# Kernel tuning notes

Measured on AMD Instinct MI355X. Metric: run time of the kernel, lower is better.

Reference implementation:

```python
import jax, jax.numpy as jnp
import numpy as np

B, KLEN, QLEN = 16, 4096, 1
D_MODEL, HEADS, KERNELS = 1024, 8, 10
DIM = D_MODEL // HEADS  # 128
SCALE = 0.02


def setup_inputs() -> dict:
    key = jax.random.key(0)
    ks = jax.random.split(key, 12)
    return {
        "query": jax.random.normal(ks[0], (B, QLEN, D_MODEL), jnp.float32),
        "key_in": jax.random.normal(ks[1], (B, KLEN, D_MODEL), jnp.float32),
        "value": jax.random.normal(ks[2], (B, KLEN, D_MODEL), jnp.float32),
        "prev_align": jax.random.uniform(ks[3], (B, HEADS, KLEN), jnp.float32),
        # learned params
        "conv_w": jax.random.normal(ks[4], (KERNELS, HEADS, 3), jnp.float32) * SCALE,   # OIH, k=3
        "conv_b": jnp.zeros((KERNELS,), jnp.float32),
        "w_u": jax.random.normal(ks[5], (KERNELS, DIM), jnp.float32) * SCALE,
        "w_q": jax.random.normal(ks[6], (D_MODEL, HEADS * DIM), jnp.float32) * SCALE,
        "w_v": jax.random.normal(ks[7], (D_MODEL, HEADS * DIM), jnp.float32) * SCALE,
        "bias": jax.random.uniform(ks[8], (DIM,), jnp.float32, minval=-0.1, maxval=0.1),
        "score_w": jax.random.normal(ks[9], (DIM,), jnp.float32) * SCALE,
        "score_b": jnp.zeros((), jnp.float32),
    }


def reference(query, key_in, value, prev_align, conv_w, conv_b, w_u, w_q, w_v, bias, score_w, score_b):
    b, k_len = key_in.shape[0], key_in.shape[1]
    # location features: conv1d over k_len with heads as channels -> [B, KERNELS, k_len]
    loc = jax.lax.conv_general_dilated(
        prev_align, conv_w, window_strides=(1,), padding=[(1, 1)],
        dimension_numbers=("NCH", "OIH", "NCH")) + conv_b[None, :, None]
    loc_energy = jnp.tanh(jnp.einsum("bck,cd->bkd", loc, w_u))  # [B, k_len, DIM]
    # projections split into heads
    q = jnp.einsum("bqf,fe->bqe", query, w_q).reshape(b, QLEN, HEADS, DIM).transpose(0, 2, 1, 3)   # [B,H,1,DIM]
    k = jnp.einsum("bkf,fe->bke", key_in, w_v).reshape(b, k_len, HEADS, DIM).transpose(0, 2, 1, 3)  # [B,H,K,DIM]
    v = value.reshape(b, k_len, HEADS, DIM).transpose(0, 2, 1, 3)                                   # [B,H,K,DIM]
    # additive energy (q_len==1 broadcasts over keys)
    e = jnp.tanh(k + q + loc_energy[:, None] + bias)            # [B,H,K,DIM]
    score = jnp.einsum("bhkd,d->bhk", e, score_w) + score_b    # [B,H,K]
    align = jax.nn.softmax(score, axis=-1)
    context = jnp.einsum("bhk,bhkd->bhd", align, v).reshape(b * HEADS, DIM)
    return context, align
```

## Files before the change

### kernel.cpp

```cpp
#include <hip/hip_runtime.h>
#include <hip/hip_bf16.h>
#include <cstdint>

typedef __attribute__((ext_vector_type(8))) short bf16x8;
typedef __attribute__((ext_vector_type(4))) float f32x4;
typedef __attribute__((ext_vector_type(8))) unsigned short u16x8;
typedef __attribute__((ext_vector_type(4))) unsigned int u32x4;

__device__ __forceinline__ unsigned short f2bf(float f) {
    unsigned int u = __float_as_uint(f);
    unsigned int r = (u + 0x7fffu + ((u >> 16) & 1u)) >> 16;
    return (unsigned short)r;
}

__device__ __forceinline__ float tanh_fast(float x) {
    return 1.0f - 2.0f / (__expf(2.0f * x) + 1.0f);
}

#define GLDS(SRC, DST) __builtin_amdgcn_global_load_lds(                         \
        (const __attribute__((address_space(1))) void*)(SRC),                    \
        (__attribute__((address_space(3))) void*)(DST), 16, 0, 0)

__global__ __launch_bounds__(256) void wv_tile_kernel(
        const float* __restrict__ wv, unsigned short* __restrict__ out) {
    __shared__ float tile[32][129];
    const int h = blockIdx.x;
    const int kt = blockIdx.y;
    const int t = threadIdx.x;
    for (int i = t; i < 1024; i += 256) {
        const int fl = i >> 5;
        const int e4 = (i & 31) * 4;
        const float4 v = *reinterpret_cast<const float4*>(
            wv + (size_t)(kt * 32 + fl) * 1024 + h * 128 + e4);
        tile[fl][e4 + 0] = v.x; tile[fl][e4 + 1] = v.y;
        tile[fl][e4 + 2] = v.z; tile[fl][e4 + 3] = v.w;
    }
    __syncthreads();
#pragma unroll
    for (int cc2 = 0; cc2 < 2; ++cc2) {
        const int c = cc2 * 256 + t;
        const int cb = c >> 6, kg = (c >> 4) & 3, ccl = c & 15;
        const int e_local = cb * 16 + ccl;
        u16x8 u;
#pragma unroll
        for (int jj = 0; jj < 8; ++jj) u[jj] = f2bf(tile[kg * 8 + jj][e_local]);
        *reinterpret_cast<u16x8*>(out + (((size_t)h * 32 + kt) * 512 + c) * 8) = u;
    }
}

__global__ __launch_bounds__(128) void qproj_kernel(
        const float* __restrict__ query, const float* __restrict__ w_q,
        float* __restrict__ ws_q) {
    __shared__ float qs[1024];
    int bh = blockIdx.x;
    int b = bh >> 3, h = bh & 7;
    int t = threadIdx.x;
    for (int i = t; i < 1024; i += 128) qs[i] = query[(size_t)b * 1024 + i];
    __syncthreads();
    float acc = 0.f;
    const float* wcol = w_q + h * 128 + t;
    for (int f = 0; f < 1024; ++f) acc += qs[f] * wcol[(size_t)f * 1024];
    ws_q[(size_t)bh * 128 + t] = acc;
}

__global__ __launch_bounds__(256) void loc_conv_kernel(
        const float* __restrict__ pa, const float* __restrict__ conv_w,
        const float* __restrict__ conv_b, float* __restrict__ ws_loc) {
    __shared__ float pas[8][258];
    __shared__ float cw[240];
    __shared__ float cb[16];
    int b = blockIdx.x, k0 = blockIdx.y * 256;
    int t = threadIdx.x;
    for (int i = t; i < 8 * 258; i += 256) {
        int hh = i / 258, kk = i % 258;
        int gk = k0 + kk - 1;
        pas[hh][kk] = (gk >= 0 && gk < 4096) ? pa[((size_t)(b * 8 + hh)) * 4096 + gk] : 0.f;
    }
    if (t < 240) cw[t] = conv_w[t];
    if (t < 10) cb[t] = conv_b[t];
    __syncthreads();
#pragma unroll
    for (int c = 0; c < 10; ++c) {
        float acc = cb[c];
#pragma unroll
        for (int hh = 0; hh < 8; ++hh) {
            acc += pas[hh][t] * cw[(c * 8 + hh) * 3 + 0]
                 + pas[hh][t + 1] * cw[(c * 8 + hh) * 3 + 1]
                 + pas[hh][t + 2] * cw[(c * 8 + hh) * 3 + 2];
        }
        ws_loc[((size_t)(b * 10 + c)) * 4096 + k0 + t] = acc;
    }
}

__global__ __launch_bounds__(256) void loc_energy_kernel(
        const float* __restrict__ ws_loc, const float* __restrict__ w_u,
        float* __restrict__ le) {
    __shared__ float loc_s[10][128];
    __shared__ float wu_s[10][128];
    const int b = blockIdx.x, k0 = blockIdx.y * 128;
    const int t = threadIdx.x;
    for (int i = t; i < 1280; i += 256) {
        const int c = i >> 7, r = i & 127;
        loc_s[c][r] = ws_loc[((size_t)(b * 10 + c)) * 4096 + k0 + r];
        wu_s[c][r] = w_u[i];
    }
    __syncthreads();
    const int k = t >> 1;
    const int d0 = (t & 1) * 64;
    float lc[10];
#pragma unroll
    for (int c = 0; c < 10; ++c) lc[c] = loc_s[c][k];
    float* dst = le + ((size_t)(b * 4096) + k0 + k) * 128 + d0;
#pragma unroll
    for (int dd = 0; dd < 64; dd += 4) {
        float4 o;
#pragma unroll
        for (int jj = 0; jj < 4; ++jj) {
            float s = 0.f;
#pragma unroll
            for (int c = 0; c < 10; ++c) s += lc[c] * wu_s[c][d0 + dd + jj];
            ((float*)&o)[jj] = tanh_fast(s);
        }
        *reinterpret_cast<float4*>(dst + dd) = o;
    }
}

#define NT 32
__global__ __launch_bounds__(512) void gemm_score_kernel(
        const float* __restrict__ key_in, const unsigned short* __restrict__ wvT_tiled,
        const float* __restrict__ le,
        const float* __restrict__ ws_q, const float* __restrict__ bias,
        const float* __restrict__ score_w, const float* __restrict__ score_b,
        float* __restrict__ align_out) {
    __shared__ __align__(16) unsigned short As[2][4096];
    __shared__ __align__(16) unsigned short Bs[2][8192];
    __shared__ float qb_sm[256], sw_sm[128];
    __shared__ float partial[128][4];

    const int t = threadIdx.x;
    const int lane = t & 63, wid = t >> 6;
    const int wm = wid >> 2;
    const int wn = wid & 3;

    const int fid = blockIdx.x;
    const int x = fid & 7, j = fid >> 3;
    const int bm = x * 64 + (j >> 2);
    const int hp = j & 3;
    const int b = bm >> 5;
    const int kk0 = (bm & 31) << 7;

    if (t < 256) {
        const int hh = t >> 7, d = t & 127;
        qb_sm[t] = ws_q[(size_t)(b * 8 + hp * 2 + hh) * 128 + d] + bias[d];
        if (t < 128) sw_sm[t] = score_w[t];
    }

    const int r_ = t >> 2, ks = t & 3;
    const float* aRow = key_in + ((size_t)(b * 4096 + kk0) + r_) * 1024 + ks * 8;
    const int cW = (t >> 6) * 64 + ks * 16 + (r_ & 15);
    const int dst0 = (cW ^ (ks | ((ks & 1) << 2))) * 8;

    const int kgR = lane >> 4;
    const int laneSwz = lane ^ (kgR | ((kgR & 1) << 2));

    const unsigned short* bT = wvT_tiled
        + (size_t)(hp * 2 + (t >> 8)) * 131072 + (t & 255) * 8;
    const int dstB = (t >> 8) * 4096 + (t & 255) * 8;

    float4 st0, st1;

#define LOADA(KT) {                                                               \
        const float* p_ = aRow + (KT) * 32;                                       \
        st0 = *reinterpret_cast<const float4*>(p_);                               \
        st1 = *reinterpret_cast<const float4*>(p_ + 4); }

#define WRITEA(BUF) {                                                             \
        __hip_bfloat162 h0_ = __float22bfloat162_rn({st0.x, st0.y});              \
        __hip_bfloat162 h1_ = __float22bfloat162_rn({st0.z, st0.w});              \
        __hip_bfloat162 h2_ = __float22bfloat162_rn({st1.x, st1.y});              \
        __hip_bfloat162 h3_ = __float22bfloat162_rn({st1.z, st1.w});              \
        u32x4 u_;                                                                 \
        u_[0] = *reinterpret_cast<unsigned int*>(&h0_);                           \
        u_[1] = *reinterpret_cast<unsigned int*>(&h1_);                           \
        u_[2] = *reinterpret_cast<unsigned int*>(&h2_);                           \
        u_[3] = *reinterpret_cast<unsigned int*>(&h3_);                           \
        *reinterpret_cast<u32x4*>(&As[BUF][dst0]) = u_; }

#define STAGE_B(BUF, KT) {                                                        \
        GLDS(bT + (size_t)(KT) * 4096, &Bs[BUF][dstB]);                           \
        GLDS(bT + (size_t)(KT) * 4096 + 2048, &Bs[BUF][dstB + 2048]); }

    f32x4 acc[4][4] = {};

    LOADA(0);
    STAGE_B(0, 0);
    WRITEA(0);
    LOADA(1);
    __syncthreads();

    for (int kt = 0; kt < NT; ++kt) {
        const int cur = kt & 1;
        if (kt < NT - 1) {
            STAGE_B(cur ^ 1, kt + 1);
            WRITEA(cur ^ 1);
        }
        if (kt < NT - 2) LOADA(kt + 2);
        bf16x8 af[4], bg[4];
#pragma unroll
        for (int mf = 0; mf < 4; ++mf)
            af[mf] = *reinterpret_cast<const bf16x8*>(
                &As[cur][((wm * 4 + mf) * 64 + laneSwz) * 8]);
#pragma unroll
        for (int nf = 0; nf < 4; ++nf)
            bg[nf] = *reinterpret_cast<const bf16x8*>(
                &Bs[cur][(wn >> 1) * 4096 + ((wn & 1) * 4 + nf) * 512 + lane * 8]);
#pragma unroll
        for (int mf = 0; mf < 4; ++mf)
#pragma unroll
            for (int nf = 0; nf < 4; ++nf)
                acc[mf][nf] = __builtin_amdgcn_mfma_f32_16x16x32_bf16(
                    af[mf], bg[nf], acc[mf][nf], 0, 0, 0);
        __syncthreads();
    }

    const float K2 = 2.8853900817779268f;
    const float sb = score_b[0];
    const int g = lane >> 4;
    float kqb[4], swv[4];
#pragma unroll
    for (int nf = 0; nf < 4; ++nf) {
        const int d128 = (wn & 1) * 64 + nf * 16 + (lane & 15);
        kqb[nf] = qb_sm[(wn >> 1) * 128 + d128] * K2;
        swv[nf] = sw_sm[d128];
    }
    const float* leB = le + ((size_t)(b * 4096 + kk0) + wm * 64 + g * 4) * 128
                       + (wn & 1) * 64 + (lane & 15);

#pragma unroll
    for (int mf = 0; mf < 4; ++mf) {
        float lv[16];
#pragma unroll
        for (int jj = 0; jj < 4; ++jj)
#pragma unroll
            for (int nf = 0; nf < 4; ++nf)
                lv[jj * 4 + nf] = leB[(size_t)(mf * 16 + jj) * 128 + nf * 16];
#pragma unroll
        for (int jj = 0; jj < 4; ++jj) {
            const int row_l = wm * 64 + mf * 16 + g * 4 + jj;
            float sum = 0.f;
#pragma unroll
            for (int nf = 0; nf < 4; ++nf) {
                const float m = fmaf(K2, lv[jj * 4 + nf], kqb[nf]);
                const float tt = fmaf(K2, acc[mf][nf][jj], m);
                const float y = __builtin_amdgcn_exp2f(tt);
                const float r = fmaf(-2.0f, __builtin_amdgcn_rcpf(y + 1.0f), 1.0f);
                sum = fmaf(r, swv[nf], sum);
            }
            sum += __shfl_xor(sum, 1);
            sum += __shfl_xor(sum, 2);
            sum += __shfl_xor(sum, 4);
            sum += __shfl_xor(sum, 8);
            if ((lane & 15) == 0) partial[row_l][wn] = sum;
        }
    }
    __syncthreads();
    if (t < 256) {
        const int r = t >> 1, hh = t & 1;
        const float sc = partial[r][hh * 2] + partial[r][hh * 2 + 1] + sb;
        align_out[(size_t)(b * 8 + hp * 2 + hh) * 4096 + kk0 + r] = sc;
    }
}

__global__ __launch_bounds__(256) void softmax_kernel(float* __restrict__ align_o) {
    const int bh = blockIdx.x;
    float* row = align_o + (size_t)bh * 4096;
    const int t = threadIdx.x;
    float v[16];
    float m = -1e30f;
#pragma unroll
    for (int i = 0; i < 16; ++i) {
        v[i] = row[i * 256 + t];
        m = fmaxf(m, v[i]);
    }
#pragma unroll
    for (int off = 32; off; off >>= 1) m = fmaxf(m, __shfl_xor(m, off));
    __shared__ float sm[4], ss[4];
    const int wid = t >> 6;
    if ((t & 63) == 0) sm[wid] = m;
    __syncthreads();
    m = fmaxf(fmaxf(sm[0], sm[1]), fmaxf(sm[2], sm[3]));
    float s = 0.f;
#pragma unroll
    for (int i = 0; i < 16; ++i) {
        v[i] = __expf(v[i] - m);
        s += v[i];
    }
#pragma unroll
    for (int off = 32; off; off >>= 1) s += __shfl_xor(s, off);
    if ((t & 63) == 0) ss[wid] = s;
    __syncthreads();
    s = ss[0] + ss[1] + ss[2] + ss[3];
    const float inv = 1.f / s;
#pragma unroll
    for (int i = 0; i < 16; ++i) row[i * 256 + t] = v[i] * inv;
}

__global__ __launch_bounds__(256) void ctx_partial_kernel(
        const float* __restrict__ value, const float* __restrict__ align_o,
        float* __restrict__ pctx) {
    const int s = blockIdx.x;
    const int bh = blockIdx.y;
    const int b = bh >> 3, h = bh & 7;
    const int t = threadIdx.x;
    const int d4 = (t & 31) * 4;
    const int kg = t >> 5;
    const float* arow = align_o + (size_t)bh * 4096 + s * 128;
    const float* vbase = value + ((size_t)(b * 4096 + s * 128)) * 1024 + h * 128 + d4;
    float4 acc = {0.f, 0.f, 0.f, 0.f};
    for (int i = 0; i < 16; ++i) {
        const int kk = i * 8 + kg;
        const float a = arow[kk];
        const float4 v = *reinterpret_cast<const float4*>(vbase + (size_t)kk * 1024);
        acc.x += a * v.x; acc.y += a * v.y; acc.z += a * v.z; acc.w += a * v.w;
    }
    __shared__ float sm2[8][128];
    *reinterpret_cast<float4*>(&sm2[kg][d4]) = acc;
    __syncthreads();
    if (t < 128) {
        float s0 = 0.f;
#pragma unroll
        for (int gg = 0; gg < 8; ++gg) s0 += sm2[gg][t];
        pctx[((size_t)bh * 32 + s) * 128 + t] = s0;
    }
}

__global__ __launch_bounds__(128) void ctx_reduce_kernel(
        const float* __restrict__ pctx, float* __restrict__ out) {
    const int bh = blockIdx.x;
    const int t = threadIdx.x;
    float acc = 0.f;
    for (int s2 = 0; s2 < 32; ++s2) acc += pctx[((size_t)bh * 32 + s2) * 128 + t];
    out[(size_t)bh * 128 + t] = acc;
}

extern "C" void kernel_launch(void* const* d_in, const int* in_sizes, int n_in,
                              void* d_out, int out_size, void* d_ws, size_t ws_size,
                              hipStream_t stream) {
    const float* query   = (const float*)d_in[0];
    const float* key_in  = (const float*)d_in[1];
    const float* value   = (const float*)d_in[2];
    const float* pa      = (const float*)d_in[3];
    const float* conv_w  = (const float*)d_in[4];
    const float* conv_b  = (const float*)d_in[5];
    const float* w_u     = (const float*)d_in[6];
    const float* w_q     = (const float*)d_in[7];
    const float* w_v     = (const float*)d_in[8];
    const float* bias    = (const float*)d_in[9];
    const float* score_w = (const float*)d_in[10];
    const float* score_b = (const float*)d_in[11];

    float* out = (float*)d_out;
    float* ctx_out = out;
    float* align_out = out + 16384;

    char* ws = (char*)d_ws;
    const size_t OFF_Q    = 0;
    const size_t OFF_LOC  = 65536;
    const size_t OFF_WVT  = OFF_LOC + 2621440;
    const size_t OFF_PCTX = OFF_WVT + 2097152;
    const size_t OFF_LE   = OFF_PCTX + 2097152;

    float* ws_q            = (float*)(ws + OFF_Q);
    float* ws_loc          = (float*)(ws + OFF_LOC);
    unsigned short* ws_wvT = (unsigned short*)(ws + OFF_WVT);
    float* ws_pctx         = (float*)(ws + OFF_PCTX);
    float* ws_le           = (float*)(ws + OFF_LE);

    hipLaunchKernelGGL(wv_tile_kernel, dim3(8, 32), dim3(256), 0, stream, w_v, ws_wvT);
    hipLaunchKernelGGL(qproj_kernel, dim3(128), dim3(128), 0, stream, query, w_q, ws_q);
    hipLaunchKernelGGL(loc_conv_kernel, dim3(16, 16), dim3(256), 0, stream, pa, conv_w, conv_b, ws_loc);
    hipLaunchKernelGGL(loc_energy_kernel, dim3(16, 32), dim3(256), 0, stream, ws_loc, w_u, ws_le);
    hipLaunchKernelGGL(gemm_score_kernel, dim3(2048), dim3(512), 0, stream,
                       key_in, ws_wvT, ws_le, ws_q, bias, score_w, score_b, align_out);
    hipLaunchKernelGGL(softmax_kernel, dim3(128), dim3(256), 0, stream, align_out);
    hipLaunchKernelGGL(ctx_partial_kernel, dim3(32, 128), dim3(256), 0, stream, value, align_out, ws_pctx);
    hipLaunchKernelGGL(ctx_reduce_kernel, dim3(128), dim3(128), 0, stream, ws_pctx, ctx_out);
}
```

Baseline: 320.1 us.

## Shrink GEMM-score block to four waves with wider per-wave N tiles

```diff
diff --git a/kernel.cpp b/kernel.cpp
--- a/kernel.cpp
+++ b/kernel.cpp
@@ -48,19 +48,19 @@
     }
 }
 
-__global__ __launch_bounds__(128) void qproj_kernel(
+__global__ __launch_bounds__(1024) void qproj_kernel(
         const float* __restrict__ query, const float* __restrict__ w_q,
         float* __restrict__ ws_q) {
     __shared__ float qs[1024];
-    int bh = blockIdx.x;
-    int b = bh >> 3, h = bh & 7;
-    int t = threadIdx.x;
-    for (int i = t; i < 1024; i += 128) qs[i] = query[(size_t)b * 1024 + i];
+    const int b = blockIdx.x;
+    const int t = threadIdx.x;
+    qs[t] = query[(size_t)b * 1024 + t];
     __syncthreads();
     float acc = 0.f;
-    const float* wcol = w_q + h * 128 + t;
-    for (int f = 0; f < 1024; ++f) acc += qs[f] * wcol[(size_t)f * 1024];
-    ws_q[(size_t)bh * 128 + t] = acc;
+    const float* w = w_q + t;
+#pragma unroll 8
+    for (int f = 0; f < 1024; ++f) acc = fmaf(qs[f], w[(size_t)f * 1024], acc);
+    ws_q[(size_t)b * 1024 + t] = acc;
 }
 
 __global__ __launch_bounds__(256) void loc_conv_kernel(
@@ -126,7 +126,7 @@
 }
 
 #define NT 32
-__global__ __launch_bounds__(512) void gemm_score_kernel(
+__global__ __launch_bounds__(256) void gemm_score_kernel(
         const float* __restrict__ key_in, const unsigned short* __restrict__ wvT_tiled,
         const float* __restrict__ le,
         const float* __restrict__ ws_q, const float* __restrict__ bias,
@@ -135,12 +135,11 @@
     __shared__ __align__(16) unsigned short As[2][4096];
     __shared__ __align__(16) unsigned short Bs[2][8192];
     __shared__ float qb_sm[256], sw_sm[128];
-    __shared__ float partial[128][4];
 
     const int t = threadIdx.x;
     const int lane = t & 63, wid = t >> 6;
-    const int wm = wid >> 2;
-    const int wn = wid & 3;
+    const int wm = wid >> 1;
+    const int wn = wid & 1;
 
     const int fid = blockIdx.x;
     const int x = fid & 7, j = fid >> 3;
@@ -149,48 +148,57 @@
     const int b = bm >> 5;
     const int kk0 = (bm & 31) << 7;
 
-    if (t < 256) {
-        const int hh = t >> 7, d = t & 127;
-        qb_sm[t] = ws_q[(size_t)(b * 8 + hp * 2 + hh) * 128 + d] + bias[d];
-        if (t < 128) sw_sm[t] = score_w[t];
-    }
-
-    const int r_ = t >> 2, ks = t & 3;
-    const float* aRow = key_in + ((size_t)(b * 4096 + kk0) + r_) * 1024 + ks * 8;
-    const int cW = (t >> 6) * 64 + ks * 16 + (r_ & 15);
-    const int dst0 = (cW ^ (ks | ((ks & 1) << 2))) * 8;
-
-    const int kgR = lane >> 4;
-    const int laneSwz = lane ^ (kgR | ((kgR & 1) << 2));
-
-    const unsigned short* bT = wvT_tiled
-        + (size_t)(hp * 2 + (t >> 8)) * 131072 + (t & 255) * 8;
-    const int dstB = (t >> 8) * 4096 + (t & 255) * 8;
-
-    float4 st0, st1;
+    qb_sm[t] = ws_q[(size_t)(b * 8 + hp * 2 + (t >> 7)) * 128 + (t & 127)] + bias[t & 127];
+    if (t < 128) sw_sm[t] = score_w[t];
+
+    const int r_ = t >> 1, ks = t & 1;
+    const float* aRow = key_in + ((size_t)(b * 4096 + kk0) + r_) * 1024 + ks * 16;
+    const int rowblk = r_ >> 4, row15 = r_ & 15;
+    const int dstA0 = (rowblk * 64 + ks * 32 + (row15 ^ (ks * 4))) * 8;
+
+    const int laneSwz = lane ^ (((lane >> 4) & 2) << 1);
+
+    const unsigned short* bT0 = wvT_tiled + (size_t)(hp * 2) * 131072 + t * 8;
+    const unsigned short* bT1 = wvT_tiled + (size_t)(hp * 2 + 1) * 131072 + t * 8;
+    const int dstB = t * 8;
+
+    float4 st0, st1, st2, st3;
 
 #define LOADA(KT) {                                                               \
         const float* p_ = aRow + (KT) * 32;                                       \
         st0 = *reinterpret_cast<const float4*>(p_);                               \
-        st1 = *reinterpret_cast<const float4*>(p_ + 4); }
+        st1 = *reinterpret_cast<const float4*>(p_ + 4);                           \
+        st2 = *reinterpret_cast<const float4*>(p_ + 8);                           \
+        st3 = *reinterpret_cast<const float4*>(p_ + 12); }
 
 #define WRITEA(BUF) {                                                             \
         __hip_bfloat162 h0_ = __float22bfloat162_rn({st0.x, st0.y});              \
         __hip_bfloat162 h1_ = __float22bfloat162_rn({st0.z, st0.w});              \
         __hip_bfloat162 h2_ = __float22bfloat162_rn({st1.x, st1.y});              \
         __hip_bfloat162 h3_ = __float22bfloat162_rn({st1.z, st1.w});              \
-        u32x4 u_;                                                                 \
-        u_[0] = *reinterpret_cast<unsigned int*>(&h0_);                           \
-        u_[1] = *reinterpret_cast<unsigned int*>(&h1_);                           \
-        u_[2] = *reinterpret_cast<unsigned int*>(&h2_);                           \
-        u_[3] = *reinterpret_cast<unsigned int*>(&h3_);                           \
-        *reinterpret_cast<u32x4*>(&As[BUF][dst0]) = u_; }
+        __hip_bfloat162 h4_ = __float22bfloat162_rn({st2.x, st2.y});              \
+        __hip_bfloat162 h5_ = __float22bfloat162_rn({st2.z, st2.w});              \
+        __hip_bfloat162 h6_ = __float22bfloat162_rn({st3.x, st3.y});              \
+        __hip_bfloat162 h7_ = __float22bfloat162_rn({st3.z, st3.w});              \
+        u32x4 ua_, ub_;                                                           \
+        ua_[0] = *reinterpret_cast<unsigned int*>(&h0_);                          \
+        ua_[1] = *reinterpret_cast<unsigned int*>(&h1_);                          \
+        ua_[2] = *reinterpret_cast<unsigned int*>(&h2_);                          \
+        ua_[3] = *reinterpret_cast<unsigned int*>(&h3_);                          \
+        ub_[0] = *reinterpret_cast<unsigned int*>(&h4_);                          \
+        ub_[1] = *reinterpret_cast<unsigned int*>(&h5_);                          \
+        ub_[2] = *reinterpret_cast<unsigned int*>(&h6_);                          \
+        ub_[3] = *reinterpret_cast<unsigned int*>(&h7_);                          \
+        *reinterpret_cast<u32x4*>(&As[BUF][dstA0]) = ua_;                         \
+        *reinterpret_cast<u32x4*>(&As[BUF][dstA0 + 128]) = ub_; }
 
 #define STAGE_B(BUF, KT) {                                                        \
-        GLDS(bT + (size_t)(KT) * 4096, &Bs[BUF][dstB]);                           \
-        GLDS(bT + (size_t)(KT) * 4096 + 2048, &Bs[BUF][dstB + 2048]); }
-
-    f32x4 acc[4][4] = {};
+        GLDS(bT0 + (size_t)(KT) * 4096,        &Bs[BUF][dstB]);                   \
+        GLDS(bT0 + (size_t)(KT) * 4096 + 2048, &Bs[BUF][dstB + 2048]);            \
+        GLDS(bT1 + (size_t)(KT) * 4096,        &Bs[BUF][dstB + 4096]);            \
+        GLDS(bT1 + (size_t)(KT) * 4096 + 2048, &Bs[BUF][dstB + 6144]); }
+
+    f32x4 acc[4][8] = {};
 
     LOADA(0);
     STAGE_B(0, 0);
@@ -205,19 +213,19 @@
             WRITEA(cur ^ 1);
         }
         if (kt < NT - 2) LOADA(kt + 2);
-        bf16x8 af[4], bg[4];
+        bf16x8 af[4], bg[8];
 #pragma unroll
         for (int mf = 0; mf < 4; ++mf)
             af[mf] = *reinterpret_cast<const bf16x8*>(
                 &As[cur][((wm * 4 + mf) * 64 + laneSwz) * 8]);
 #pragma unroll
-        for (int nf = 0; nf < 4; ++nf)
+        for (int nf = 0; nf < 8; ++nf)
             bg[nf] = *reinterpret_cast<const bf16x8*>(
-                &Bs[cur][(wn >> 1) * 4096 + ((wn & 1) * 4 + nf) * 512 + lane * 8]);
+                &Bs[cur][wn * 4096 + (nf * 64 + lane) * 8]);
 #pragma unroll
         for (int mf = 0; mf < 4; ++mf)
 #pragma unroll
-            for (int nf = 0; nf < 4; ++nf)
+            for (int nf = 0; nf < 8; ++nf)
                 acc[mf][nf] = __builtin_amdgcn_mfma_f32_16x16x32_bf16(
                     af[mf], bg[nf], acc[mf][nf], 0, 0, 0);
         __syncthreads();
@@ -226,31 +234,32 @@
     const float K2 = 2.8853900817779268f;
     const float sb = score_b[0];
     const int g = lane >> 4;
-    float kqb[4], swv[4];
-#pragma unroll
-    for (int nf = 0; nf < 4; ++nf) {
-        const int d128 = (wn & 1) * 64 + nf * 16 + (lane & 15);
-        kqb[nf] = qb_sm[(wn >> 1) * 128 + d128] * K2;
-        swv[nf] = sw_sm[d128];
-    }
-    const float* leB = le + ((size_t)(b * 4096 + kk0) + wm * 64 + g * 4) * 128
-                       + (wn & 1) * 64 + (lane & 15);
+    const int l15 = lane & 15;
+    float kqb[8], swv[8];
+#pragma unroll
+    for (int nf = 0; nf < 8; ++nf) {
+        const int d = nf * 16 + l15;
+        kqb[nf] = qb_sm[wn * 128 + d] * K2;
+        swv[nf] = sw_sm[d];
+    }
+    const float* leB = le + ((size_t)(b * 4096 + kk0) + wm * 64 + g * 4) * 128 + l15;
+    float* aout = align_out + (size_t)(b * 8 + hp * 2 + wn) * 4096 + kk0;
 
 #pragma unroll
     for (int mf = 0; mf < 4; ++mf) {
-        float lv[16];
+        float lv[32];
 #pragma unroll
         for (int jj = 0; jj < 4; ++jj)
 #pragma unroll
-            for (int nf = 0; nf < 4; ++nf)
-                lv[jj * 4 + nf] = leB[(size_t)(mf * 16 + jj) * 128 + nf * 16];
+            for (int nf = 0; nf < 8; ++nf)
+                lv[jj * 8 + nf] = leB[(size_t)(mf * 16 + jj) * 128 + nf * 16];
 #pragma unroll
         for (int jj = 0; jj < 4; ++jj) {
             const int row_l = wm * 64 + mf * 16 + g * 4 + jj;
             float sum = 0.f;
 #pragma unroll
-            for (int nf = 0; nf < 4; ++nf) {
-                const float m = fmaf(K2, lv[jj * 4 + nf], kqb[nf]);
+            for (int nf = 0; nf < 8; ++nf) {
+                const float m = fmaf(K2, lv[jj * 8 + nf], kqb[nf]);
                 const float tt = fmaf(K2, acc[mf][nf][jj], m);
                 const float y = __builtin_amdgcn_exp2f(tt);
                 const float r = fmaf(-2.0f, __builtin_amdgcn_rcpf(y + 1.0f), 1.0f);
@@ -260,14 +269,8 @@
             sum += __shfl_xor(sum, 2);
             sum += __shfl_xor(sum, 4);
             sum += __shfl_xor(sum, 8);
-            if ((lane & 15) == 0) partial[row_l][wn] = sum;
+            if (l15 == 0) aout[row_l] = sum + sb;
         }
-    }
-    __syncthreads();
-    if (t < 256) {
-        const int r = t >> 1, hh = t & 1;
-        const float sc = partial[r][hh * 2] + partial[r][hh * 2 + 1] + sb;
-        align_out[(size_t)(b * 8 + hp * 2 + hh) * 4096 + kk0 + r] = sc;
     }
 }
 
@@ -377,10 +380,10 @@
     float* ws_le           = (float*)(ws + OFF_LE);
 
     hipLaunchKernelGGL(wv_tile_kernel, dim3(8, 32), dim3(256), 0, stream, w_v, ws_wvT);
-    hipLaunchKernelGGL(qproj_kernel, dim3(128), dim3(128), 0, stream, query, w_q, ws_q);
+    hipLaunchKernelGGL(qproj_kernel, dim3(16), dim3(1024), 0, stream, query, w_q, ws_q);
     hipLaunchKernelGGL(loc_conv_kernel, dim3(16, 16), dim3(256), 0, stream, pa, conv_w, conv_b, ws_loc);
     hipLaunchKernelGGL(loc_energy_kernel, dim3(16, 32), dim3(256), 0, stream, ws_loc, w_u, ws_le);
-    hipLaunchKernelGGL(gemm_score_kernel, dim3(2048), dim3(512), 0, stream,
+    hipLaunchKernelGGL(gemm_score_kernel, dim3(2048), dim3(256), 0, stream,
                        key_in, ws_wvT, ws_le, ws_q, bias, score_w, score_b, align_out);
     hipLaunchKernelGGL(softmax_kernel, dim3(128), dim3(256), 0, stream, align_out);
     hipLaunchKernelGGL(ctx_partial_kernel, dim3(32, 128), dim3(256), 0, stream, value, align_out, ws_pctx);
```

Result: slower. 493.3 us (+54.1%).
